# Performance work log

Hardware: AMD Instinct MI355X
Metric: run time of the kernel (lower is better)

## Reference

```python
import jax, jax.numpy as jnp
import numpy as np

B, T, C = 4, 1024, 1024
NH, L, DHR, FF = 16, 512, 64, 4096
DK = C // NH  # 64
EPS = 1e-6
NEG = -9e15


def rms_norm(x, w):
    var = jnp.mean(jnp.square(x), axis=-1, keepdims=True)
    return x * jax.lax.rsqrt(var + EPS) * w


def rope_apply(x):
    # Faithful to RoPE module: freq = t+1, pos pairs repeated, theta = exp(-2*pos/C*ln(1e4))
    b, t, c = x.shape
    xf = x.astype(jnp.float32)
    freq = jnp.arange(t, dtype=jnp.float32)[:, None] + 1.0           # [t,1]
    pos = jnp.arange(c // 2, dtype=jnp.float32)[:, None]
    pos = jnp.repeat(pos, 2, axis=-1).reshape(1, -1)                 # [1,c] -> p0,p0,p1,p1,...
    theta = jnp.exp(-2.0 * pos / c * jnp.log(10000.0))
    cos = jnp.cos(freq * theta)                                      # [t,c]
    sin = jnp.sin(freq * theta)
    x2 = xf.reshape(b, t, c // 2, 2)
    rot = jnp.stack([-x2[..., 1], x2[..., 0]], axis=-1).reshape(b, t, c)
    return (xf * cos + rot * sin).astype(x.dtype)


def setup_inputs() -> dict:
    key = jax.random.key(0)
    ks = jax.random.split(key, 12)
    s = 0.02
    return {
        "x": jax.random.normal(ks[0], (B, T, C), jnp.float32),
        "rms1": jnp.ones((C,), jnp.float32),
        "rms2": jnp.ones((C,), jnp.float32),
        "W_dkv": s * jax.random.normal(ks[1], (C, 2 * L), jnp.float32),
        "b_dkv": jnp.zeros((2 * L,), jnp.float32),
        "W_kr": s * jax.random.normal(ks[2], (2 * L, DHR), jnp.float32),
        "b_kr": jnp.zeros((DHR,), jnp.float32),
        "W_qr": s * jax.random.normal(ks[3], (2 * L, DHR * NH), jnp.float32),
        "b_qr": jnp.zeros((DHR * NH,), jnp.float32),
        "W_kv": s * jax.random.normal(ks[4], (L, 2 * C), jnp.float32),
        "b_kv": jnp.zeros((2 * C,), jnp.float32),
        "W_q": s * jax.random.normal(ks[5], (L, C), jnp.float32),
        "b_q": jnp.zeros((C,), jnp.float32),
        "W_o": s * jax.random.normal(ks[6], (C, C), jnp.float32),
        "b_o": jnp.zeros((C,), jnp.float32),
        "W_f1": s * jax.random.normal(ks[7], (C, FF), jnp.float32),
        "b_f1": jnp.zeros((FF,), jnp.float32),
        "W_f2": s * jax.random.normal(ks[8], (FF, C), jnp.float32),
        "b_f2": jnp.zeros((C,), jnp.float32),
    }


def mla(x, W_dkv, b_dkv, W_kr, b_kr, W_qr, b_qr, W_kv, b_kv, W_q, b_q, W_o, b_o):
    b, t, c = x.shape
    comp = jnp.einsum('btc,cd->btd', x, W_dkv) + b_dkv               # [B,T,2L]
    cKV, cq = jnp.split(comp, 2, axis=-1)                            # [B,T,L] each
    # RoPE branches (computed from the compressed representation, as in source)
    kR = rope_apply(jnp.einsum('btl,ld->btd', comp, W_kr) + b_kr)    # [B,T,DHR]
    qR = rope_apply(jnp.einsum('btl,ld->btd', comp, W_qr) + b_qr)    # roped over full NH*DHR dim
    qR = qR.reshape(b, t, NH, DHR).transpose(0, 2, 1, 3)             # [B,NH,T,DHR]
    kv = jnp.einsum('btl,ld->btd', cKV, W_kv) + b_kv
    k, v = jnp.split(kv, 2, axis=-1)                                 # [B,T,C] each
    q = jnp.einsum('btl,ld->btd', cq, W_q) + b_q                     # [B,T,C]
    to_heads = lambda z: z.reshape(b, t, NH, DK).transpose(0, 2, 1, 3)
    q, k, v = to_heads(q), to_heads(k), to_heads(v)                  # [B,NH,T,DK]
    q = jnp.concatenate([q, qR], axis=-1)                            # [B,NH,T,DK+DHR]
    k = jnp.concatenate([k, jnp.broadcast_to(kR[:, None], (b, NH, t, DHR))], axis=-1)
    # manual masked softmax in fp32, scale uses DK (not DK+DHR), faithful to source
    scale = 1.0 / np.sqrt(DK)
    w = jnp.einsum('bnqd,bnkd->bnqk', q.astype(jnp.float32), k.astype(jnp.float32)) * scale
    mask = jnp.tril(jnp.ones((t, t), jnp.float32))
    w = jnp.where(mask == 0, NEG, w)
    p = jax.nn.softmax(w, axis=-1)
    o = jnp.einsum('bnqk,bnkd->bnqd', p, v.astype(jnp.float32)).astype(x.dtype)
    o = o.transpose(0, 2, 1, 3).reshape(b, t, c)
    return jnp.einsum('btc,cd->btd', o, W_o) + b_o


def ffn(x, W_f1, b_f1, W_f2, b_f2):
    h = jax.nn.gelu(jnp.einsum('btc,cf->btf', x, W_f1) + b_f1)
    return jnp.einsum('btf,fc->btc', h, W_f2) + b_f2


def reference(x, rms1, rms2, W_dkv, b_dkv, W_kr, b_kr, W_qr, b_qr,
              W_kv, b_kv, W_q, b_q, W_o, b_o, W_f1, b_f1, W_f2, b_f2):
    h = x + mla(rms_norm(x, rms1), W_dkv, b_dkv, W_kr, b_kr, W_qr, b_qr,
                W_kv, b_kv, W_q, b_q, W_o, b_o)
    out = h + ffn(rms_norm(h, rms2), W_f1, b_f1, W_f2, b_f2)
    return out
```

## Files before the change

### kernel.cpp

```cpp
#include <hip/hip_runtime.h>

typedef unsigned int u32;
typedef unsigned short u16;
typedef __bf16 bf16x8 __attribute__((ext_vector_type(8)));
typedef float f32x4 __attribute__((ext_vector_type(4)));

#define B_ 4
#define T_ 1024
#define C_ 1024
#define NH_ 16
#define L_ 512
#define DHR_ 64
#define FF_ 4096

typedef __attribute__((address_space(3))) u32 as3_u32;
typedef __attribute__((address_space(1))) u32 as1_u32;

__device__ __forceinline__ void gld16(const u16* g, u16* l) {
  __builtin_amdgcn_global_load_lds((const as1_u32*)g, (as3_u32*)l, 16, 0, 0);
}

__device__ __forceinline__ float bf2f(u16 u) {
  union { u32 i; float f; } v; v.i = ((u32)u) << 16; return v.f;
}
__device__ __forceinline__ u16 f2bf(float f) {
  union { float f; u32 i; } v; v.f = f;
  u32 r = (v.i + 0x7FFFu + ((v.i >> 16) & 1u)) >> 16;
  return (u16)r;
}

struct TransArgs {
  const float* src[8];
  u16* dst[8];
  int R[8], C[8];
  int base[9];
  const float* x;
  const float* rmsw;
  u16* xn;
};

__global__ void pre_all(TransArgs ta) {
  const int bid = blockIdx.x;
  if (bid >= ta.base[8]) {
    const int row = bid - ta.base[8];
    const int tid = threadIdx.y * 32 + threadIdx.x;
    const float* xp = ta.x + (size_t)row * C_;
    float v[4];
#pragma unroll
    for (int i = 0; i < 4; i++) v[i] = xp[tid + 256 * i];
    float ss = v[0] * v[0] + v[1] * v[1] + v[2] * v[2] + v[3] * v[3];
#pragma unroll
    for (int o = 32; o > 0; o >>= 1) ss += __shfl_down(ss, o, 64);
    __shared__ float red[4];
    if ((tid & 63) == 0) red[tid >> 6] = ss;
    __syncthreads();
    ss = red[0] + red[1] + red[2] + red[3];
    float scale = rsqrtf(ss * (1.0f / 1024.0f) + 1e-6f);
    u16* op = ta.xn + (size_t)row * C_;
#pragma unroll
    for (int i = 0; i < 4; i++)
      op[tid + 256 * i] = f2bf(v[i] * scale * ta.rmsw[tid + 256 * i]);
    return;
  }
  __shared__ float tile[32][33];
  int w = 0;
#pragma unroll
  for (int i = 1; i < 8; i++) w += (bid >= ta.base[i]);
  const int local = bid - ta.base[w];
  const int R = ta.R[w], C = ta.C[w];
  const int ctiles = C >> 5;
  const int bx = (local % ctiles) * 32;
  const int by = (local / ctiles) * 32;
  const float* in = ta.src[w];
  u16* outp = ta.dst[w];
  const int tx = threadIdx.x, ty = threadIdx.y;
  for (int i = ty; i < 32; i += 8)
    tile[i][tx] = in[(size_t)(by + i) * C + bx + tx];
  __syncthreads();
  for (int i = ty; i < 32; i += 8)
    outp[(size_t)(bx + i) * R + by + tx] = f2bf(tile[tx][i]);
}

__global__ __launch_bounds__(256) void rmsnorm_kernel(const float* __restrict__ xin,
                                                      const float* __restrict__ w,
                                                      u16* __restrict__ outp) {
  const int row = blockIdx.x;
  const int tid = threadIdx.x;
  const float* xp = xin + (size_t)row * C_;
  float v[4];
#pragma unroll
  for (int i = 0; i < 4; i++) v[i] = xp[tid + 256 * i];
  float ss = v[0] * v[0] + v[1] * v[1] + v[2] * v[2] + v[3] * v[3];
#pragma unroll
  for (int o = 32; o > 0; o >>= 1) ss += __shfl_down(ss, o, 64);
  __shared__ float red[4];
  if ((tid & 63) == 0) red[tid >> 6] = ss;
  __syncthreads();
  ss = red[0] + red[1] + red[2] + red[3];
  float scale = rsqrtf(ss * (1.0f / 1024.0f) + 1e-6f);
  u16* op = outp + (size_t)row * C_;
#pragma unroll
  for (int i = 0; i < 4; i++)
    op[tid + 256 * i] = f2bf(v[i] * scale * w[tid + 256 * i]);
}

template<int EPI, bool NCLIP, int NT>
__device__ __forceinline__ void g_body(
    u16* As, u16* Bs,
    const u16* __restrict__ A, int lda, int aoff,
    const u16* __restrict__ BT, const float* __restrict__ bias,
    const float* __restrict__ resid, void* __restrict__ out,
    int N, int Kfull, int Klen, int m0, int n0, int koff) {
  const int tid = threadIdx.x;
  const int wave = tid >> 6, lane = tid & 63;
  const int wm = wave >> 1, wn = wave & 1;
  const int quad = lane >> 4, l15 = lane & 15;
  const int row = tid >> 2, seg = tid & 3;

  const u16* aP = A + (size_t)(m0 + row) * lda + aoff + koff + seg * 8;
  const u16* bP = BT + (size_t)(n0 + row) * Kfull + koff + seg * 8;
  u16* aL = As + row * 32 + seg * 8;
  u16* bL = Bs + row * 32 + seg * 8;
  const size_t aStep = (size_t)64 * lda;
  const size_t bStep = (size_t)64 * Kfull;

  f32x4 acc[4][NT] = {};

  for (int k0 = 0; k0 < Klen; k0 += 32) {
    gld16(aP + k0, aL);
    gld16(aP + k0 + aStep, aL + 64 * 32);
    gld16(bP + k0, bL);
    if (NT == 4) gld16(bP + k0 + bStep, bL + 64 * 32);
    __syncthreads();
    bf16x8 af[4], bfr[NT];
#pragma unroll
    for (int mt = 0; mt < 4; mt++)
      af[mt] = *(const bf16x8*)&As[(wm * 64 + mt * 16 + l15) * 32 + quad * 8];
#pragma unroll
    for (int nt = 0; nt < NT; nt++)
      bfr[nt] = *(const bf16x8*)&Bs[(wn * (NT * 16) + nt * 16 + l15) * 32 + quad * 8];
#pragma unroll
    for (int mt = 0; mt < 4; mt++)
#pragma unroll
      for (int nt = 0; nt < NT; nt++)
        acc[mt][nt] = __builtin_amdgcn_mfma_f32_16x16x32_bf16(af[mt], bfr[nt], acc[mt][nt], 0, 0, 0);
    __syncthreads();
  }

  float bvv[NT];
#pragma unroll
  for (int nt = 0; nt < NT; nt++) {
    const int gn = n0 + wn * (NT * 16) + nt * 16 + l15;
    bvv[nt] = (EPI == 4) ? 0.0f : ((NCLIP && gn >= N) ? 0.0f : bias[gn]);
  }
#pragma unroll
  for (int mt = 0; mt < 4; mt++) {
#pragma unroll
    for (int i = 0; i < 4; i++) {
      const int gm = m0 + wm * 64 + mt * 16 + quad * 4 + i;
      const size_t rowb = (size_t)gm * N;
#pragma unroll
      for (int nt = 0; nt < NT; nt++) {
        const int gn = n0 + wn * (NT * 16) + nt * 16 + l15;
        if (NCLIP && gn >= N) continue;
        const size_t oidx = rowb + gn;
        float v = acc[mt][nt][i] + bvv[nt];
        if (EPI == 2) {
          float y = 0.7978845608028654f * (v + 0.044715f * v * v * v);
          float t = __expf(fminf(2.0f * y, 80.0f));
          v = v * t / (t + 1.0f);
        }
        if (EPI == 3) v += resid[oidx];
        if (EPI == 1 || EPI == 3 || EPI == 4) ((float*)out)[oidx] = v;
        else ((u16*)out)[oidx] = f2bf(v);
      }
    }
  }
}

template<int EPI, int NT>
__global__ __launch_bounds__(256) void gemmN(
    const u16* __restrict__ A, int lda, int aoff,
    const u16* __restrict__ BT, const float* __restrict__ bias,
    const float* __restrict__ resid, void* __restrict__ out,
    int N, int K) {
  __shared__ __align__(16) u16 As[128 * 32];
  __shared__ __align__(16) u16 Bs[NT * 32 * 32];
  g_body<EPI, false, NT>(As, Bs, A, lda, aoff, BT, bias, resid, out,
                         N, K, K, blockIdx.x * 128, blockIdx.y * (NT * 32), 0);
}

__global__ __launch_bounds__(256) void gemm128_splitk(
    const u16* __restrict__ A, int lda, const u16* __restrict__ BT,
    float* __restrict__ part, int N, int Kfull, int Klen) {
  __shared__ __align__(16) u16 As[128 * 32];
  __shared__ __align__(16) u16 Bs[128 * 32];
  const int z = blockIdx.z;
  g_body<4, false, 4>(As, Bs, A, lda, 0, BT, nullptr, nullptr,
                      part + (size_t)z * 4096 * N,
                      N, Kfull, Klen, blockIdx.x * 128, blockIdx.y * 128, z * Klen);
}

__global__ __launch_bounds__(256) void f2_reduce(
    const float* __restrict__ part, const float* __restrict__ h,
    const float* __restrict__ bias, float* __restrict__ out) {
  const size_t base = (size_t)blockIdx.x * 1024;
  const size_t PS = (size_t)4096 * 1024;
#pragma unroll
  for (int i = 0; i < 4; i++) {
    const int col = threadIdx.x + 256 * i;
    out[base + col] = h[base + col] + bias[col] + part[base + col] +
                      part[PS + base + col] + part[2 * PS + base + col] +
                      part[3 * PS + base + col];
  }
}

__global__ __launch_bounds__(256) void proj_fused(
    const u16* __restrict__ comp,
    const u16* __restrict__ WT_qr, const float* __restrict__ b_qr, float* __restrict__ qr_pre,
    const u16* __restrict__ WT_kr, const float* __restrict__ b_kr, float* __restrict__ kr_pre,
    const u16* __restrict__ WT_kv, const float* __restrict__ b_kv, u16* __restrict__ kvbuf,
    const u16* __restrict__ WT_q, const float* __restrict__ b_q, u16* __restrict__ qbuf) {
  __shared__ __align__(16) u16 As[128 * 32];
  __shared__ __align__(16) u16 Bs[128 * 32];
  const int m0 = blockIdx.x * 128;
  const int ny = blockIdx.y;
  if (ny < 8)
    g_body<1, false, 4>(As, Bs, comp, 1024, 0, WT_qr, b_qr, nullptr, qr_pre, 1024, 1024, 1024, m0, ny * 128, 0);
  else if (ny == 8)
    g_body<1, true, 4>(As, Bs, comp, 1024, 0, WT_kr, b_kr, nullptr, kr_pre, 64, 1024, 1024, m0, 0, 0);
  else if (ny < 25)
    g_body<0, false, 4>(As, Bs, comp, 1024, 0, WT_kv, b_kv, nullptr, kvbuf, 2048, 512, 512, m0, (ny - 9) * 128, 0);
  else
    g_body<0, false, 4>(As, Bs, comp, 1024, 512, WT_q, b_q, nullptr, qbuf, 1024, 512, 512, m0, (ny - 25) * 128, 0);
}

__global__ __launch_bounds__(256) void rope_vtrans(
    const u16* __restrict__ qb, const float* __restrict__ qr_pre,
    const u16* __restrict__ kvb, const float* __restrict__ kr_pre,
    u16* __restrict__ Qf, u16* __restrict__ Kf, u16* __restrict__ Vf) {
  __shared__ u16 tile[64][72];
  if (blockIdx.x >= 4096) {
    const int bid2 = blockIdx.x - 4096;
    const int bh = bid2 & 63, t0 = (bid2 >> 6) * 64;
    const int b = bh >> 4, h = bh & 15;
    const int r = threadIdx.x >> 2, seg = (threadIdx.x & 3) * 16;
    const u16* src = &kvb[((size_t)(b * 1024) + t0 + r) * 2048 + 1024 + h * 64 + seg];
    *(uint4*)&tile[r][seg] = *(const uint4*)src;
    *(uint4*)&tile[r][seg + 8] = *(const uint4*)(src + 8);
    __syncthreads();
    const int d = threadIdx.x >> 2, ts = (threadIdx.x & 3) * 16;
    u16 tmp[16];
#pragma unroll
    for (int j = 0; j < 16; j++) tmp[j] = tile[ts + j][d];
    u16* dst = &Vf[((size_t)bh * 64 + d) * 1024 + t0 + ts];
    *(uint4*)dst = *(uint4*)tmp;
    *(uint4*)(dst + 8) = *(uint4*)(tmp + 8);
    return;
  }
  const int bt = blockIdx.x;
  const int b = bt >> 10, t = bt & 1023;
  const float freq = (float)(t + 1);
  for (int idx = threadIdx.x; idx < 2048; idx += 256) {
    const int h = idx >> 7, d = idx & 127;
    const size_t dst = (((size_t)(b * 16 + h)) * T_ + t) * 128 + d;
    u16 qv, kvv;
    if (d < 64) {
      qv = qb[(size_t)bt * C_ + h * 64 + d];
      kvv = kvb[(size_t)bt * 2048 + h * 64 + d];
    } else {
      const int dd = d - 64;
      {
        const int g = h * 64 + dd;
        const int p = g >> 1;
        const float theta = __expf(-(float)(2 * p) * (9.210340372f / 1024.0f));
        float s, c;
        sincosf(freq * theta, &s, &c);
        const float x0 = qr_pre[(size_t)bt * 1024 + (p << 1)];
        const float x1 = qr_pre[(size_t)bt * 1024 + (p << 1) + 1];
        qv = f2bf((g & 1) ? (x1 * c + x0 * s) : (x0 * c - x1 * s));
      }
      {
        const int p = dd >> 1;
        const float theta = __expf(-(float)(2 * p) * (9.210340372f / 64.0f));
        float s, c;
        sincosf(freq * theta, &s, &c);
        const float x0 = kr_pre[(size_t)bt * 64 + (p << 1)];
        const float x1 = kr_pre[(size_t)bt * 64 + (p << 1) + 1];
        kvv = f2bf((dd & 1) ? (x1 * c + x0 * s) : (x0 * c - x1 * s));
      }
    }
    Qf[dst] = qv;
    Kf[dst] = kvv;
  }
}

#define KSTR 136
#define VSTR 72

__device__ __forceinline__ void attn_tile(
    u16* Ks, u16* Vt, u16* Ps,
    const u16* __restrict__ Qf, const u16* __restrict__ Kf,
    const u16* __restrict__ Vf, u16* __restrict__ attn_o,
    int b, int h, int qt) {
  const int tid = threadIdx.x;
  const int wave = tid >> 6, lane = tid & 63;
  const int quad = lane >> 4, l15 = lane & 15;
  const int q0 = qt * 64;
  const size_t bh = (size_t)(b * 16 + h);

  bf16x8 qfrag[4];
  {
    const u16* qb = &Qf[(bh * T_ + q0 + wave * 16 + l15) * 128 + quad * 8];
#pragma unroll
    for (int kc = 0; kc < 4; kc++) qfrag[kc] = *(const bf16x8*)(qb + kc * 32);
  }

  f32x4 acc_o[4] = {};
  float m_i[4], l_i[4];
#pragma unroll
  for (int i = 0; i < 4; i++) { m_i[i] = -3.0e38f; l_i[i] = 0.0f; }

  const int kr_ = tid >> 3, kcs = (tid & 7) * 16;
  const int vd = tid >> 2, vts = (tid & 3) * 16;
  u16* Pw = Ps + wave * 16 * VSTR;

  for (int kt = 0; kt <= qt; kt++) {
    __syncthreads();
    {
      const u16* s0 = &Kf[(bh * T_ + kt * 64 + kr_) * 128 + kcs];
      const u16* s1 = s0 + 32 * 128;
      *(uint4*)&Ks[kr_ * KSTR + kcs] = *(const uint4*)s0;
      *(uint4*)&Ks[kr_ * KSTR + kcs + 8] = *(const uint4*)(s0 + 8);
      *(uint4*)&Ks[(kr_ + 32) * KSTR + kcs] = *(const uint4*)s1;
      *(uint4*)&Ks[(kr_ + 32) * KSTR + kcs + 8] = *(const uint4*)(s1 + 8);
      const u16* vs = &Vf[(bh * 64 + vd) * 1024 + kt * 64 + vts];
      *(uint4*)&Vt[vd * VSTR + vts] = *(const uint4*)vs;
      *(uint4*)&Vt[vd * VSTR + vts + 8] = *(const uint4*)(vs + 8);
    }
    __syncthreads();

    f32x4 acc_s[4] = {};
#pragma unroll
    for (int kc = 0; kc < 4; kc++) {
#pragma unroll
      for (int ng = 0; ng < 4; ng++) {
        bf16x8 bb = *(const bf16x8*)&Ks[(ng * 16 + l15) * KSTR + kc * 32 + quad * 8];
        acc_s[ng] = __builtin_amdgcn_mfma_f32_16x16x32_bf16(qfrag[kc], bb, acc_s[ng], 0, 0, 0);
      }
    }

    float sv[4][4];
#pragma unroll
    for (int ng = 0; ng < 4; ng++)
#pragma unroll
      for (int i = 0; i < 4; i++) {
        float s = acc_s[ng][i] * 0.125f;
        if (kt == qt && (ng * 16 + l15) > (wave * 16 + quad * 4 + i)) s = -3.0e38f;
        sv[ng][i] = s;
      }

    float alpha[4], mx[4];
#pragma unroll
    for (int i = 0; i < 4; i++) {
      float m = fmaxf(fmaxf(sv[0][i], sv[1][i]), fmaxf(sv[2][i], sv[3][i]));
#pragma unroll
      for (int off = 1; off < 16; off <<= 1) m = fmaxf(m, __shfl_xor(m, off, 64));
      float mn = fmaxf(m_i[i], m);
      alpha[i] = __expf(m_i[i] - mn);
      m_i[i] = mn;
      mx[i] = mn;
    }
    float rs[4] = {0.f, 0.f, 0.f, 0.f};
#pragma unroll
    for (int ng = 0; ng < 4; ng++)
#pragma unroll
      for (int i = 0; i < 4; i++) {
        float p = __expf(sv[ng][i] - mx[i]);
        rs[i] += p;
        Pw[(quad * 4 + i) * VSTR + ng * 16 + l15] = f2bf(p);
      }
#pragma unroll
    for (int i = 0; i < 4; i++) {
      float r = rs[i];
#pragma unroll
      for (int off = 1; off < 16; off <<= 1) r += __shfl_xor(r, off, 64);
      l_i[i] = l_i[i] * alpha[i] + r;
    }

#pragma unroll
    for (int ng = 0; ng < 4; ng++)
#pragma unroll
      for (int i = 0; i < 4; i++) acc_o[ng][i] *= alpha[i];
#pragma unroll
    for (int kc = 0; kc < 2; kc++) {
      bf16x8 a = *(const bf16x8*)&Pw[l15 * VSTR + kc * 32 + quad * 8];
#pragma unroll
      for (int ng = 0; ng < 4; ng++) {
        bf16x8 bb = *(const bf16x8*)&Vt[(ng * 16 + l15) * VSTR + kc * 32 + quad * 8];
        acc_o[ng] = __builtin_amdgcn_mfma_f32_16x16x32_bf16(a, bb, acc_o[ng], 0, 0, 0);
      }
    }
  }

  float linv[4];
#pragma unroll
  for (int i = 0; i < 4; i++) linv[i] = 1.0f / l_i[i];
#pragma unroll
  for (int ng = 0; ng < 4; ng++)
#pragma unroll
    for (int i = 0; i < 4; i++) {
      const int qrow = q0 + wave * 16 + quad * 4 + i;
      attn_o[((size_t)(b * T_) + qrow) * C_ + h * 64 + ng * 16 + l15] =
          f2bf(acc_o[ng][i] * linv[i]);
    }
}

__global__ __launch_bounds__(256) void attn_mfma(
    const u16* __restrict__ Qf, const u16* __restrict__ Kf,
    const u16* __restrict__ Vf, u16* __restrict__ attn_o) {
  __shared__ __align__(16) u16 Ks[64 * KSTR];
  __shared__ __align__(16) u16 Vt[64 * VSTR];
  __shared__ __align__(16) u16 Ps[4 * 16 * VSTR];
  const int j = blockIdx.x & 7;
  const int h = (blockIdx.x >> 3) & 15;
  const int b = blockIdx.x >> 7;
  attn_tile(Ks, Vt, Ps, Qf, Kf, Vf, attn_o, b, h, 15 - j);
  attn_tile(Ks, Vt, Ps, Qf, Kf, Vf, attn_o, b, h, j);
}

extern "C" void kernel_launch(void* const* d_in, const int* in_sizes, int n_in,
                              void* d_out, int out_size, void* d_ws, size_t ws_size,
                              hipStream_t stream) {
  const float* x = (const float*)d_in[0];
  const float* rms1 = (const float*)d_in[1];
  const float* rms2 = (const float*)d_in[2];
  const float* W_dkv = (const float*)d_in[3];
  const float* b_dkv = (const float*)d_in[4];
  const float* W_kr = (const float*)d_in[5];
  const float* b_kr = (const float*)d_in[6];
  const float* W_qr = (const float*)d_in[7];
  const float* b_qr = (const float*)d_in[8];
  const float* W_kv = (const float*)d_in[9];
  const float* b_kv = (const float*)d_in[10];
  const float* W_q = (const float*)d_in[11];
  const float* b_q = (const float*)d_in[12];
  const float* W_o = (const float*)d_in[13];
  const float* b_o = (const float*)d_in[14];
  const float* W_f1 = (const float*)d_in[15];
  const float* b_f1 = (const float*)d_in[16];
  const float* W_f2 = (const float*)d_in[17];
  const float* b_f2 = (const float*)d_in[18];
  float* out = (float*)d_out;

  char* ws = (char*)d_ws;
  size_t off = 0;
  auto alloc = [&](size_t bytes) -> void* {
    void* p = ws + off;
    off += (bytes + 255) & ~(size_t)255;
    return p;
  };
  u16* WT_dkv = (u16*)alloc((size_t)1024 * 1024 * 2);
  u16* WT_kr  = (u16*)alloc((size_t)128 * 1024 * 2);
  u16* WT_qr  = (u16*)alloc((size_t)1024 * 1024 * 2);
  u16* WT_kv  = (u16*)alloc((size_t)2048 * 512 * 2);
  u16* WT_q   = (u16*)alloc((size_t)1024 * 512 * 2);
  u16* WT_o   = (u16*)alloc((size_t)1024 * 1024 * 2);
  u16* WT_f1  = (u16*)alloc((size_t)4096 * 1024 * 2);
  u16* WT_f2  = (u16*)alloc((size_t)1024 * 4096 * 2);
  u16* xn1    = (u16*)alloc((size_t)4096 * 1024 * 2);
  u16* comp   = (u16*)alloc((size_t)4096 * 1024 * 2);
  float* kr_pre = (float*)alloc((size_t)4096 * 64 * 4);
  float* qr_pre = (float*)alloc((size_t)4096 * 1024 * 4);
  u16* kvbuf  = (u16*)alloc((size_t)4096 * 2048 * 2);
  u16* qbuf   = (u16*)alloc((size_t)4096 * 1024 * 2);
  u16* Qf     = (u16*)alloc((size_t)64 * 1024 * 128 * 2);
  u16* Kf     = (u16*)alloc((size_t)64 * 1024 * 128 * 2);
  u16* Vf     = (u16*)alloc((size_t)64 * 64 * 1024 * 2);
  u16* attn_o = (u16*)alloc((size_t)4096 * 1024 * 2);
  alloc((size_t)4096 * 1024 * 4);
  float* hbuf = (float*)alloc((size_t)4096 * 1024 * 4);
  u16* hn     = (u16*)alloc((size_t)4096 * 1024 * 2);
  u16* hid    = (u16*)alloc((size_t)4096 * 4096 * 2);
  float* partial = (float*)Qf;

  TransArgs ta;
  const float* srcs[8] = {W_dkv, W_kr, W_qr, W_kv, W_q, W_o, W_f1, W_f2};
  u16* dsts[8] = {WT_dkv, WT_kr, WT_qr, WT_kv, WT_q, WT_o, WT_f1, WT_f2};
  const int Rs[8] = {1024, 1024, 1024, 512, 512, 1024, 1024, 4096};
  const int Cs[8] = {1024, 64, 1024, 2048, 1024, 1024, 4096, 1024};
  int acc_t = 0;
  for (int i = 0; i < 8; i++) {
    ta.src[i] = srcs[i]; ta.dst[i] = dsts[i]; ta.R[i] = Rs[i]; ta.C[i] = Cs[i];
    ta.base[i] = acc_t;
    acc_t += (Rs[i] >> 5) * (Cs[i] >> 5);
  }
  ta.base[8] = acc_t;
  ta.x = x; ta.rmsw = rms1; ta.xn = xn1;
  pre_all<<<acc_t + 4096, dim3(32, 8), 0, stream>>>(ta);

  gemmN<0, 2><<<dim3(32, 16), 256, 0, stream>>>(xn1, 1024, 0, WT_dkv, b_dkv, nullptr, comp, 1024, 1024);

  proj_fused<<<dim3(32, 33), 256, 0, stream>>>(comp,
      WT_qr, b_qr, qr_pre, WT_kr, b_kr, kr_pre,
      WT_kv, b_kv, kvbuf, WT_q, b_q, qbuf);

  rope_vtrans<<<4096 + 1024, 256, 0, stream>>>(qbuf, qr_pre, kvbuf, kr_pre, Qf, Kf, Vf);

  attn_mfma<<<B_ * NH_ * 8, 256, 0, stream>>>(Qf, Kf, Vf, attn_o);

  gemmN<3, 2><<<dim3(32, 16), 256, 0, stream>>>(attn_o, 1024, 0, WT_o, b_o, x, hbuf, 1024, 1024);

  rmsnorm_kernel<<<4096, 256, 0, stream>>>(hbuf, rms2, hn);

  gemmN<2, 4><<<dim3(32, 32), 256, 0, stream>>>(hn, 1024, 0, WT_f1, b_f1, nullptr, hid, 4096, 1024);

  gemm128_splitk<<<dim3(32, 8, 4), 256, 0, stream>>>(hid, 4096, WT_f2, partial, 1024, 4096, 1024);
  f2_reduce<<<4096, 256, 0, stream>>>(partial, hbuf, b_f2, out);
}
```

Measured before the change: 445.0 us.

## Double GEMM K-tile to 64 with XOR-swizzled LDS and halve FFN2 split-K

The shared GEMM body now stages 64-wide K slices per iteration instead of 32, which halves the number of barrier pairs per tile. LDS rows are XOR-swizzled by row index to avoid bank conflicts on the wider 128-byte rows. The FFN2 split-K factor drops from 4 to 2, so there is less partial-sum traffic and less reduction work, but fewer blocks are available to fill the GPU. LDS use per block doubles, which may lower occupancy.

```diff
diff --git a/kernel.cpp b/kernel.cpp
--- a/kernel.cpp
+++ b/kernel.cpp
@@ -115,35 +115,47 @@
   const int wave = tid >> 6, lane = tid & 63;
   const int wm = wave >> 1, wn = wave & 1;
   const int quad = lane >> 4, l15 = lane & 15;
-  const int row = tid >> 2, seg = tid & 3;
-
-  const u16* aP = A + (size_t)(m0 + row) * lda + aoff + koff + seg * 8;
-  const u16* bP = BT + (size_t)(n0 + row) * Kfull + koff + seg * 8;
-  u16* aL = As + row * 32 + seg * 8;
-  u16* bL = Bs + row * 32 + seg * 8;
-  const size_t aStep = (size_t)64 * lda;
-  const size_t bStep = (size_t)64 * Kfull;
+  const int srow = tid >> 3;
+  const int gseg = (tid & 7) ^ (srow & 7);
+
+  const u16* aP = A + (size_t)(m0 + srow) * lda + aoff + koff + gseg * 8;
+  const u16* bP = BT + (size_t)(n0 + srow) * Kfull + koff + gseg * 8;
+  u16* aL = As + tid * 8;
+  u16* bL = Bs + tid * 8;
+  const size_t aStep = (size_t)32 * lda;
+  const size_t bStep = (size_t)32 * Kfull;
 
   f32x4 acc[4][NT] = {};
 
-  for (int k0 = 0; k0 < Klen; k0 += 32) {
-    gld16(aP + k0, aL);
-    gld16(aP + k0 + aStep, aL + 64 * 32);
-    gld16(bP + k0, bL);
-    if (NT == 4) gld16(bP + k0 + bStep, bL + 64 * 32);
+  for (int k0 = 0; k0 < Klen; k0 += 64) {
+#pragma unroll
+    for (int c = 0; c < 4; c++)
+      gld16(aP + k0 + c * aStep, aL + c * 32 * 64);
+#pragma unroll
+    for (int c = 0; c < NT; c++)
+      gld16(bP + k0 + c * bStep, bL + c * 32 * 64);
     __syncthreads();
-    bf16x8 af[4], bfr[NT];
-#pragma unroll
-    for (int mt = 0; mt < 4; mt++)
-      af[mt] = *(const bf16x8*)&As[(wm * 64 + mt * 16 + l15) * 32 + quad * 8];
-#pragma unroll
-    for (int nt = 0; nt < NT; nt++)
-      bfr[nt] = *(const bf16x8*)&Bs[(wn * (NT * 16) + nt * 16 + l15) * 32 + quad * 8];
-#pragma unroll
-    for (int mt = 0; mt < 4; mt++)
-#pragma unroll
-      for (int nt = 0; nt < NT; nt++)
-        acc[mt][nt] = __builtin_amdgcn_mfma_f32_16x16x32_bf16(af[mt], bfr[nt], acc[mt][nt], 0, 0, 0);
+#pragma unroll
+    for (int kh = 0; kh < 2; kh++) {
+      bf16x8 af[4], bfr[NT];
+#pragma unroll
+      for (int mt = 0; mt < 4; mt++) {
+        const int r = wm * 64 + mt * 16 + l15;
+        const int p = (kh * 4 + quad) ^ (r & 7);
+        af[mt] = *(const bf16x8*)&As[r * 64 + p * 8];
+      }
+#pragma unroll
+      for (int nt = 0; nt < NT; nt++) {
+        const int r = wn * (NT * 16) + nt * 16 + l15;
+        const int p = (kh * 4 + quad) ^ (r & 7);
+        bfr[nt] = *(const bf16x8*)&Bs[r * 64 + p * 8];
+      }
+#pragma unroll
+      for (int mt = 0; mt < 4; mt++)
+#pragma unroll
+        for (int nt = 0; nt < NT; nt++)
+          acc[mt][nt] = __builtin_amdgcn_mfma_f32_16x16x32_bf16(af[mt], bfr[nt], acc[mt][nt], 0, 0, 0);
+    }
     __syncthreads();
   }
 
@@ -184,8 +196,8 @@
     const u16* __restrict__ BT, const float* __restrict__ bias,
     const float* __restrict__ resid, void* __restrict__ out,
     int N, int K) {
-  __shared__ __align__(16) u16 As[128 * 32];
-  __shared__ __align__(16) u16 Bs[NT * 32 * 32];
+  __shared__ __align__(16) u16 As[128 * 64];
+  __shared__ __align__(16) u16 Bs[NT * 32 * 64];
   g_body<EPI, false, NT>(As, Bs, A, lda, aoff, BT, bias, resid, out,
                          N, K, K, blockIdx.x * 128, blockIdx.y * (NT * 32), 0);
 }
@@ -193,8 +205,8 @@
 __global__ __launch_bounds__(256) void gemm128_splitk(
     const u16* __restrict__ A, int lda, const u16* __restrict__ BT,
     float* __restrict__ part, int N, int Kfull, int Klen) {
-  __shared__ __align__(16) u16 As[128 * 32];
-  __shared__ __align__(16) u16 Bs[128 * 32];
+  __shared__ __align__(16) u16 As[128 * 64];
+  __shared__ __align__(16) u16 Bs[128 * 64];
   const int z = blockIdx.z;
   g_body<4, false, 4>(As, Bs, A, lda, 0, BT, nullptr, nullptr,
                       part + (size_t)z * 4096 * N,
@@ -210,8 +222,7 @@
   for (int i = 0; i < 4; i++) {
     const int col = threadIdx.x + 256 * i;
     out[base + col] = h[base + col] + bias[col] + part[base + col] +
-                      part[PS + base + col] + part[2 * PS + base + col] +
-                      part[3 * PS + base + col];
+                      part[PS + base + col];
   }
 }
 
@@ -221,8 +232,8 @@
     const u16* __restrict__ WT_kr, const float* __restrict__ b_kr, float* __restrict__ kr_pre,
     const u16* __restrict__ WT_kv, const float* __restrict__ b_kv, u16* __restrict__ kvbuf,
     const u16* __restrict__ WT_q, const float* __restrict__ b_q, u16* __restrict__ qbuf) {
-  __shared__ __align__(16) u16 As[128 * 32];
-  __shared__ __align__(16) u16 Bs[128 * 32];
+  __shared__ __align__(16) u16 As[128 * 64];
+  __shared__ __align__(16) u16 Bs[128 * 64];
   const int m0 = blockIdx.x * 128;
   const int ny = blockIdx.y;
   if (ny < 8)
@@ -478,7 +489,6 @@
   u16* Kf     = (u16*)alloc((size_t)64 * 1024 * 128 * 2);
   u16* Vf     = (u16*)alloc((size_t)64 * 64 * 1024 * 2);
   u16* attn_o = (u16*)alloc((size_t)4096 * 1024 * 2);
-  alloc((size_t)4096 * 1024 * 4);
   float* hbuf = (float*)alloc((size_t)4096 * 1024 * 4);
   u16* hn     = (u16*)alloc((size_t)4096 * 1024 * 2);
   u16* hid    = (u16*)alloc((size_t)4096 * 4096 * 2);
@@ -515,6 +525,6 @@
 
   gemmN<2, 4><<<dim3(32, 32), 256, 0, stream>>>(hn, 1024, 0, WT_f1, b_f1, nullptr, hid, 4096, 1024);
 
-  gemm128_splitk<<<dim3(32, 8, 4), 256, 0, stream>>>(hid, 4096, WT_f2, partial, 1024, 4096, 1024);
+  gemm128_splitk<<<dim3(32, 8, 2), 256, 0, stream>>>(hid, 4096, WT_f2, partial, 1024, 4096, 2048);
   f2_reduce<<<4096, 256, 0, stream>>>(partial, hbuf, b_f2, out);
 }
```

After: 421.2 us. 5.4% less time.
